# Optimization experiments

Hardware: AMD Instinct MI355X
Metric: run time of the kernel (lower is better)

## Reference

```python
import jax, jax.numpy as jnp
import numpy as np

B, H, S, D = 2, 8, 2048, 64


def setup_inputs() -> dict:
    key = jax.random.key(0)
    kq, kk, kv, km = jax.random.split(key, 4)
    Q = jax.random.normal(kq, (B, H, S, D), dtype=jnp.float32)
    K = jax.random.normal(kk, (B, H, S, D), dtype=jnp.float32)
    V = jax.random.normal(kv, (B, H, S, D), dtype=jnp.float32)
    attn_mask = jax.random.randint(km, (B, H, S, S), 0, 2).astype(jnp.bool_)
    return {"Q": Q, "K": K, "V": V, "attn_mask": attn_mask}


def reference(Q, K, V, attn_mask):
    # a = Q K^T / sqrt(D)
    scale = 1.0 / jnp.sqrt(jnp.float32(Q.shape[-1]))
    a = jnp.einsum("bhqd,bhkd->bhqk", Q, K) * scale
    a = jnp.where(attn_mask, jnp.float32(-1e9), a)
    attn_p = jax.nn.softmax(a, axis=-1)
    # FAITHFUL to source bug: uses pre-softmax scores `a`, not attn_p
    attn_v = jnp.einsum("bhqk,bhkd->bhqd", a, V)
    return attn_v, attn_p
```

## Files before the change

kernel.cpp:

```cpp
#include <hip/hip_runtime.h>
#include <hip/hip_bf16.h>


#define SS   2048
#define DD   64
#define NT   8
#define MASK_B 0
#define K_B    4224
#define V_B    6400
#define ARENA_H 8960
#define KST 68
#define VST 20
#define FST 132

#define OV_F4 524288
#define ZB_F4 8192
#define PK_OFF  131072
#define PK_BYTES ((size_t)16*2048*16*16)

typedef _Float16 half4_t  __attribute__((ext_vector_type(4)));
typedef _Float16 half2_t  __attribute__((ext_vector_type(2)));
typedef short    short4_t __attribute__((ext_vector_type(4)));
typedef float    float4_t __attribute__((ext_vector_type(4)));
typedef int      int2_t   __attribute__((ext_vector_type(2)));
typedef unsigned uint2_t  __attribute__((ext_vector_type(2)));
typedef unsigned long long ulong2_t __attribute__((ext_vector_type(2)));

static __device__ __forceinline__ unsigned short f2bf_u(float f) {
  __hip_bfloat16 h = __float2bfloat16(f);
  return __builtin_bit_cast(unsigned short, h);
}
static __device__ __forceinline__ unsigned packh2(float a, float b) {
  union { half2_t h; unsigned u; } c;
  c.h.x = (_Float16)a; c.h.y = (_Float16)b;
  return c.u;
}

extern "C" __global__ __launch_bounds__(256)
void zero_k(float4_t* __restrict__ Ov, float4_t* __restrict__ Zb)
{
  const int i = blockIdx.x * 256 + threadIdx.x;
  const float4_t z = (float4_t){0.f, 0.f, 0.f, 0.f};
  if (i < OV_F4) Ov[i] = z;
  else           Zb[i - OV_F4] = z;
}

extern "C" __global__ __launch_bounds__(256, 1)
void attn_z_k(const float* __restrict__ Qg, const float* __restrict__ Kg,
              const float* __restrict__ Vg, const int* __restrict__ Mg,
              float* __restrict__ Og, float* __restrict__ Zg,
              unsigned long long* __restrict__ Wp, int do_pack)
{
  __shared__ alignas(16) unsigned short arena[ARENA_H];

  const int wg  = blockIdx.x;
  const int xcd = wg & 7;
  const int ii  = wg >> 3;
  const int bh  = 2 * xcd + (ii >> 9);
  const int rem = ii & 511;
  const int qg  = rem >> 4;
  const int kc  = rem & 15;

  const int tid  = threadIdx.x;
  const int w    = tid >> 6;
  const int lane = tid & 63;
  const int g    = lane >> 4;
  const int ql   = lane & 15;

  const int q0 = qg * 64 + w * 16;
  const int k0 = kc * 128;

  const int krow = 4 * w + (lane >> 4);
  const int kcol = 4 * (lane & 15);

  const float* Kst = Kg + ((size_t)bh * SS + k0 + krow) * DD + kcol;
  const float* Vst = Vg + ((size_t)bh * SS + k0 + krow) * DD + kcol;

  float4_t qr[4];
  #pragma unroll
  for (int c = 0; c < 4; ++c)
    qr[c] = *(const float4_t*)(Qg + ((size_t)bh * SS + q0 + ql) * DD + 16 * c + 4 * g);

  int2_t mrow[16];
  #pragma unroll
  for (int r = 0; r < 16; ++r)
    mrow[r] = __builtin_nontemporal_load(
        (const int2_t*)(Mg + ((size_t)bh * SS + q0 + r) * SS + k0) + lane);

  float4_t kreg = *(const float4_t*)(Kst);
  float4_t vreg = *(const float4_t*)(Vst);

  half4_t qf[4];
  #pragma unroll
  for (int c = 0; c < 4; ++c) {
    half4_t h; h.x=(_Float16)qr[c].x; h.y=(_Float16)qr[c].y;
               h.z=(_Float16)qr[c].z; h.w=(_Float16)qr[c].w;
    qf[c] = h;
  }

  #pragma unroll
  for (int r = 0; r < 16; ++r) {
    const unsigned short pk =
        (unsigned short)((mrow[r].x ? 1u : 0u) | ((mrow[r].y ? 1u : 0u) << 8));
    arena[MASK_B + w * 1056 + r * 66 + lane] = pk;
    const unsigned long long ev = __ballot(mrow[r].x != 0);
    const unsigned long long od = __ballot(mrow[r].y != 0);
    if (do_pack && lane == 0) {
      ulong2_t pm; pm.x = ev; pm.y = od;
      *(ulong2_t*)&Wp[(((size_t)bh * SS + q0 + r) * 16 + kc) * 2] = pm;
    }
  }

  {
    half4_t kh; kh.x=(_Float16)kreg.x; kh.y=(_Float16)kreg.y;
                kh.z=(_Float16)kreg.z; kh.w=(_Float16)kreg.w;
    *(half4_t*)&arena[K_B + krow * KST + kcol] = kh;
    arena[V_B + (kcol + 0) * VST + krow] = f2bf_u(vreg.x);
    arena[V_B + (kcol + 1) * VST + krow] = f2bf_u(vreg.y);
    arena[V_B + (kcol + 2) * VST + krow] = f2bf_u(vreg.z);
    arena[V_B + (kcol + 3) * VST + krow] = f2bf_u(vreg.w);
  }
  __syncthreads();

  float4_t accO[4];
  #pragma unroll
  for (int c = 0; c < 4; ++c) accO[c] = (float4_t){0.f, 0.f, 0.f, 0.f};
  float zs = 0.f;

  const unsigned short NEGu = 0xCE6Eu;

  #pragma unroll
  for (int t = 0; t < NT; ++t) {
    const int s = t & 1;

    if (t + 1 < NT) {
      kreg = *(const float4_t*)(Kst + (size_t)16 * (t + 1) * DD);
      vreg = *(const float4_t*)(Vst + (size_t)16 * (t + 1) * DD);
    }

    half4_t kf[4];
    #pragma unroll
    for (int c = 0; c < 4; ++c)
      kf[c] = *(const half4_t*)&arena[K_B + s * 1088 + ql * KST + 16 * c + 4 * g];

    short4_t vf[4];
    #pragma unroll
    for (int c = 0; c < 4; ++c)
      vf[c] = *(const short4_t*)&arena[V_B + s * 1280 + (16 * c + ql) * VST + 4 * g];

    const unsigned mdw = *(const unsigned*)((const unsigned char*)arena
                          + 2u * (MASK_B + w * 1056 + ql * 66) + 16 * t + 4 * g);

    float4_t acc = (float4_t){0.f, 0.f, 0.f, 0.f};
    #pragma unroll
    for (int c = 0; c < 4; ++c)
      acc = __builtin_amdgcn_mfma_f32_16x16x16f16(kf[c], qf[c], acc, 0, 0, 0);

    const float a0 = (mdw & 0x000000ffu) ? -1e9f : acc.x * 0.125f;
    const float a1 = (mdw & 0x0000ff00u) ? -1e9f : acc.y * 0.125f;
    const float a2 = (mdw & 0x00ff0000u) ? -1e9f : acc.z * 0.125f;
    const float a3 = (mdw & 0xff000000u) ? -1e9f : acc.w * 0.125f;

    const float e0 = __expf(a0), e1 = __expf(a1);
    const float e2 = __expf(a2), e3 = __expf(a3);
    zs += (e0 + e1) + (e2 + e3);

    short4_t af;
    af.x = (short)((mdw & 0x000000ffu) ? NEGu : 0);
    af.y = (short)((mdw & 0x0000ff00u) ? NEGu : 0);
    af.z = (short)((mdw & 0x00ff0000u) ? NEGu : 0);
    af.w = (short)((mdw & 0xff000000u) ? NEGu : 0);
    #pragma unroll
    for (int c = 0; c < 4; ++c)
      accO[c] = __builtin_amdgcn_mfma_f32_16x16x16bf16_1k(af, vf[c], accO[c], 0, 0, 0);

    if (t + 1 < NT) {
      const int s2 = s ^ 1;
      half4_t kh; kh.x=(_Float16)kreg.x; kh.y=(_Float16)kreg.y;
                  kh.z=(_Float16)kreg.z; kh.w=(_Float16)kreg.w;
      *(half4_t*)&arena[K_B + s2 * 1088 + krow * KST + kcol] = kh;
      arena[V_B + s2 * 1280 + (kcol + 0) * VST + krow] = f2bf_u(vreg.x);
      arena[V_B + s2 * 1280 + (kcol + 1) * VST + krow] = f2bf_u(vreg.y);
      arena[V_B + s2 * 1280 + (kcol + 2) * VST + krow] = f2bf_u(vreg.z);
      arena[V_B + s2 * 1280 + (kcol + 3) * VST + krow] = f2bf_u(vreg.w);
    }
    __syncthreads();
  }

  zs += __shfl_xor(zs, 16);
  zs += __shfl_xor(zs, 32);
  if (lane < 16) atomicAdd(&Zg[(size_t)bh * SS + q0 + lane], zs);

  #pragma unroll
  for (int c = 0; c < 4; ++c) {
    float* op = Og + ((size_t)bh * SS + q0 + 4 * g) * DD + 16 * c + ql;
    atomicAdd(op + 0 * DD, accO[c].x);
    atomicAdd(op + 1 * DD, accO[c].y);
    atomicAdd(op + 2 * DD, accO[c].z);
    atomicAdd(op + 3 * DD, accO[c].w);
  }
}

extern "C" __global__ __launch_bounds__(256, 1)
void attn_p_pk(const float* __restrict__ Qg, const float* __restrict__ Kg,
               const float* __restrict__ Zg, const unsigned long long* __restrict__ Wp,
               float* __restrict__ Pg)
{
  __shared__ alignas(16) unsigned short arena[ARENA_H];

  const int wg  = blockIdx.x;
  const int xcd = wg & 7;
  const int ii  = wg >> 3;
  const int bh  = 2 * xcd + (ii >> 9);
  const int rem = ii & 511;
  const int qg  = rem >> 4;
  const int kc  = rem & 15;

  const int tid  = threadIdx.x;
  const int w    = tid >> 6;
  const int lane = tid & 63;
  const int g    = lane >> 4;
  const int ql   = lane & 15;

  const int q0 = qg * 64 + w * 16;
  const int k0 = kc * 128;

  const int krow = 4 * w + (lane >> 4);
  const int kcol = 4 * (lane & 15);

  const float* Kst = Kg + ((size_t)bh * SS + k0 + krow) * DD + kcol;

  float4_t qr[4];
  #pragma unroll
  for (int c = 0; c < 4; ++c)
    qr[c] = *(const float4_t*)(Qg + ((size_t)bh * SS + q0 + ql) * DD + 16 * c + 4 * g);

  const ulong2_t pm = *(const ulong2_t*)&Wp[(((size_t)bh * SS + q0 + ql) * 16 + kc) * 2];
  const unsigned long long ev = pm.x, od = pm.y;

  float4_t kreg = *(const float4_t*)(Kst);
  const float invZ = 1.0f / Zg[(size_t)bh * SS + q0 + ql];

  half4_t qf[4];
  #pragma unroll
  for (int c = 0; c < 4; ++c) {
    half4_t h; h.x=(_Float16)qr[c].x; h.y=(_Float16)qr[c].y;
               h.z=(_Float16)qr[c].z; h.w=(_Float16)qr[c].w;
    qf[c] = h;
  }

  {
    half4_t kh; kh.x=(_Float16)kreg.x; kh.y=(_Float16)kreg.y;
                kh.z=(_Float16)kreg.z; kh.w=(_Float16)kreg.w;
    *(half4_t*)&arena[K_B + krow * KST + kcol] = kh;
  }
  __syncthreads();

  unsigned e_dw[NT][2];

  #pragma unroll
  for (int t = 0; t < NT; ++t) {
    const int s = t & 1;

    if (t + 1 < NT)
      kreg = *(const float4_t*)(Kst + (size_t)16 * (t + 1) * DD);

    half4_t kf[4];
    #pragma unroll
    for (int c = 0; c < 4; ++c)
      kf[c] = *(const half4_t*)&arena[K_B + s * 1088 + ql * KST + 16 * c + 4 * g];

    float4_t acc = (float4_t){0.f, 0.f, 0.f, 0.f};
    #pragma unroll
    for (int c = 0; c < 4; ++c)
      acc = __builtin_amdgcn_mfma_f32_16x16x16f16(kf[c], qf[c], acc, 0, 0, 0);

    const int sh = 8 * t + 2 * g;
    const unsigned m0 = (unsigned)(ev >> sh) & 1u;
    const unsigned m1 = (unsigned)(od >> sh) & 1u;
    const unsigned m2 = (unsigned)(ev >> (sh + 1)) & 1u;
    const unsigned m3 = (unsigned)(od >> (sh + 1)) & 1u;

    const float a0 = m0 ? -1e9f : acc.x * 0.125f;
    const float a1 = m1 ? -1e9f : acc.y * 0.125f;
    const float a2 = m2 ? -1e9f : acc.z * 0.125f;
    const float a3 = m3 ? -1e9f : acc.w * 0.125f;

    const float p0 = __expf(a0) * invZ, p1 = __expf(a1) * invZ;
    const float p2 = __expf(a2) * invZ, p3 = __expf(a3) * invZ;
    e_dw[t][0] = packh2(p0, p1);
    e_dw[t][1] = packh2(p2, p3);

    if (t + 1 < NT) {
      const int s2 = s ^ 1;
      half4_t kh; kh.x=(_Float16)kreg.x; kh.y=(_Float16)kreg.y;
                  kh.z=(_Float16)kreg.z; kh.w=(_Float16)kreg.w;
      *(half4_t*)&arena[K_B + s2 * 1088 + krow * KST + kcol] = kh;
    }
    __syncthreads();
  }

  {
    unsigned short* Fw = arena + w * 2112;
    #pragma unroll
    for (int t = 0; t < NT; ++t) {
      uint2_t pk; pk.x = e_dw[t][0]; pk.y = e_dw[t][1];
      *(uint2_t*)&Fw[ql * FST + 16 * t + 4 * g] = pk;
    }
    asm volatile("s_waitcnt lgkmcnt(0)" ::: "memory");
    const size_t prow = (size_t)bh * SS + q0;
    #pragma unroll
    for (int rr = 0; rr < 8; ++rr) {
      const int row = 2 * rr + (lane >> 5);
      const half4_t ev4 = *(const half4_t*)&Fw[row * FST + 4 * (lane & 31)];
      float4_t pv;
      pv.x = (float)ev4.x; pv.y = (float)ev4.y; pv.z = (float)ev4.z; pv.w = (float)ev4.w;
      __builtin_nontemporal_store(pv, (float4_t*)(Pg + (prow + row) * SS + k0 + 4 * (lane & 31)));
    }
  }
}

extern "C" __global__ __launch_bounds__(256, 1)
void attn_p_dir(const float* __restrict__ Qg, const float* __restrict__ Kg,
                const int* __restrict__ Mg, const float* __restrict__ Zg,
                float* __restrict__ Pg)
{
  __shared__ alignas(16) unsigned short arena[ARENA_H];

  const int wg  = blockIdx.x;
  const int xcd = wg & 7;
  const int ii  = wg >> 3;
  const int bh  = 2 * xcd + (ii >> 9);
  const int rem = ii & 511;
  const int qg  = rem >> 4;
  const int kc  = rem & 15;

  const int tid  = threadIdx.x;
  const int w    = tid >> 6;
  const int lane = tid & 63;
  const int g    = lane >> 4;
  const int ql   = lane & 15;

  const int q0 = qg * 64 + w * 16;
  const int k0 = kc * 128;

  const int krow = 4 * w + (lane >> 4);
  const int kcol = 4 * (lane & 15);

  const float* Kst = Kg + ((size_t)bh * SS + k0 + krow) * DD + kcol;

  float4_t qr[4];
  #pragma unroll
  for (int c = 0; c < 4; ++c)
    qr[c] = *(const float4_t*)(Qg + ((size_t)bh * SS + q0 + ql) * DD + 16 * c + 4 * g);

  int2_t mrow[16];
  #pragma unroll
  for (int r = 0; r < 16; ++r)
    mrow[r] = *((const int2_t*)(Mg + ((size_t)bh * SS + q0 + r) * SS + k0) + lane);

  float4_t kreg = *(const float4_t*)(Kst);
  const float invZ = 1.0f / Zg[(size_t)bh * SS + q0 + ql];

  half4_t qf[4];
  #pragma unroll
  for (int c = 0; c < 4; ++c) {
    half4_t h; h.x=(_Float16)qr[c].x; h.y=(_Float16)qr[c].y;
               h.z=(_Float16)qr[c].z; h.w=(_Float16)qr[c].w;
    qf[c] = h;
  }

  #pragma unroll
  for (int r = 0; r < 16; ++r) {
    const unsigned short pk =
        (unsigned short)((mrow[r].x ? 1u : 0u) | ((mrow[r].y ? 1u : 0u) << 8));
    arena[MASK_B + w * 1056 + r * 66 + lane] = pk;
  }
  {
    half4_t kh; kh.x=(_Float16)kreg.x; kh.y=(_Float16)kreg.y;
                kh.z=(_Float16)kreg.z; kh.w=(_Float16)kreg.w;
    *(half4_t*)&arena[K_B + krow * KST + kcol] = kh;
  }
  __syncthreads();

  unsigned e_dw[NT][2];

  #pragma unroll
  for (int t = 0; t < NT; ++t) {
    const int s = t & 1;

    if (t + 1 < NT)
      kreg = *(const float4_t*)(Kst + (size_t)16 * (t + 1) * DD);

    half4_t kf[4];
    #pragma unroll
    for (int c = 0; c < 4; ++c)
      kf[c] = *(const half4_t*)&arena[K_B + s * 1088 + ql * KST + 16 * c + 4 * g];

    const unsigned mdw = *(const unsigned*)((const unsigned char*)arena
                          + 2u * (MASK_B + w * 1056 + ql * 66) + 16 * t + 4 * g);

    float4_t acc = (float4_t){0.f, 0.f, 0.f, 0.f};
    #pragma unroll
    for (int c = 0; c < 4; ++c)
      acc = __builtin_amdgcn_mfma_f32_16x16x16f16(kf[c], qf[c], acc, 0, 0, 0);

    const float a0 = (mdw & 0x000000ffu) ? -1e9f : acc.x * 0.125f;
    const float a1 = (mdw & 0x0000ff00u) ? -1e9f : acc.y * 0.125f;
    const float a2 = (mdw & 0x00ff0000u) ? -1e9f : acc.z * 0.125f;
    const float a3 = (mdw & 0xff000000u) ? -1e9f : acc.w * 0.125f;

    const float p0 = __expf(a0) * invZ, p1 = __expf(a1) * invZ;
    const float p2 = __expf(a2) * invZ, p3 = __expf(a3) * invZ;
    e_dw[t][0] = packh2(p0, p1);
    e_dw[t][1] = packh2(p2, p3);

    if (t + 1 < NT) {
      const int s2 = s ^ 1;
      half4_t kh; kh.x=(_Float16)kreg.x; kh.y=(_Float16)kreg.y;
                  kh.z=(_Float16)kreg.z; kh.w=(_Float16)kreg.w;
      *(half4_t*)&arena[K_B + s2 * 1088 + krow * KST + kcol] = kh;
    }
    __syncthreads();
  }

  {
    unsigned short* Fw = arena + w * 2112;
    #pragma unroll
    for (int t = 0; t < NT; ++t) {
      uint2_t pk; pk.x = e_dw[t][0]; pk.y = e_dw[t][1];
      *(uint2_t*)&Fw[ql * FST + 16 * t + 4 * g] = pk;
    }
    asm volatile("s_waitcnt lgkmcnt(0)" ::: "memory");
    const size_t prow = (size_t)bh * SS + q0;
    #pragma unroll
    for (int rr = 0; rr < 8; ++rr) {
      const int row = 2 * rr + (lane >> 5);
      const half4_t ev4 = *(const half4_t*)&Fw[row * FST + 4 * (lane & 31)];
      float4_t pv;
      pv.x = (float)ev4.x; pv.y = (float)ev4.y; pv.z = (float)ev4.z; pv.w = (float)ev4.w;
      __builtin_nontemporal_store(pv, (float4_t*)(Pg + (prow + row) * SS + k0 + 4 * (lane & 31)));
    }
  }
}

extern "C" void kernel_launch(void* const* d_in, const int* in_sizes, int n_in,
                              void* d_out, int out_size, void* d_ws, size_t ws_size,
                              hipStream_t stream) {
  const float* Q = (const float*)d_in[0];
  const float* K = (const float*)d_in[1];
  const float* V = (const float*)d_in[2];
  const int*   M = (const int*)d_in[3];
  float* Ov = (float*)d_out;
  float* P  = (float*)d_out + (size_t)2 * 8 * 2048 * 64;
  float* Zb = (float*)d_ws;
  unsigned long long* Wp = (unsigned long long*)((char*)d_ws + PK_OFF);
  const int packed = (ws_size >= PK_OFF + PK_BYTES) ? 1 : 0;

  zero_k<<<dim3((OV_F4 + ZB_F4) / 256), dim3(256), 0, stream>>>((float4_t*)Ov, (float4_t*)Zb);
  attn_z_k<<<dim3(8192), dim3(256), 0, stream>>>(Q, K, V, M, Ov, Zb, Wp, packed);
  if (packed)
    attn_p_pk<<<dim3(8192), dim3(256), 0, stream>>>(Q, K, Zb, Wp, P);
  else
    attn_p_dir<<<dim3(8192), dim3(256), 0, stream>>>(Q, K, M, Zb, P);
}
```

Baseline: 198.5 us.

## Restructure attn_z kernel so each wave owns its own key slice with LDS reduction

The attn_z_k kernel now gives each workgroup one 16-query tile and four waves that each process a separate 128-key slice, staging K/V per wave in a larger LDS arena with no per-step __syncthreads. Partial Z sums and output accumulators are reduced across waves in LDS before one set of global atomics. The goal is to remove per-iteration block barriers and cut global atomic traffic on O and Z by a factor of four. In exchange it uses more LDS, gives each workgroup less Q reuse, and loads K/V redundantly per wave. The remaining kernels are mostly renamed loop variables.

```diff
diff --git a/kernel.cpp b/kernel.cpp
--- a/kernel.cpp
+++ b/kernel.cpp
@@ -5,12 +5,15 @@
 #define SS   2048
 #define DD   64
 #define NT   8
+#define ZMB  0
+#define ZKB  4224
+#define ZVB  12928
+#define ZRZ  23168
+#define ZAH  23296
 #define MASK_B 0
 #define K_B    4224
-#define V_B    6400
 #define ARENA_H 8960
 #define KST 68
-#define VST 20
 #define FST 132
 
 #define OV_F4 524288
@@ -51,6 +54,192 @@
               float* __restrict__ Og, float* __restrict__ Zg,
               unsigned long long* __restrict__ Wp, int do_pack)
 {
+  __shared__ alignas(16) unsigned short arena[ZAH];
+
+  const int wg  = blockIdx.x;
+  const int xcd = wg & 7;
+  const int ii  = wg >> 3;
+  const int bh  = 2 * xcd + (ii >> 9);
+  const int rem = ii & 511;
+  const int qg  = rem >> 2;
+  const int kc  = rem & 3;
+
+  const int tid  = threadIdx.x;
+  const int w    = tid >> 6;
+  const int lane = tid & 63;
+  const int g    = lane >> 4;
+  const int ql   = lane & 15;
+
+  const int q0 = qg * 16;
+  const int kw = kc * 512 + w * 128;
+
+  const int srow = lane >> 4;
+  const int scol = 4 * (lane & 15);
+
+  const float* Kst = Kg + ((size_t)bh * SS + kw) * DD;
+  const float* Vst = Vg + ((size_t)bh * SS + kw) * DD;
+
+  float4_t qr[4];
+  #pragma unroll
+  for (int d = 0; d < 4; ++d)
+    qr[d] = *(const float4_t*)(Qg + ((size_t)bh * SS + q0 + ql) * DD + 16 * d + 4 * g);
+
+  int2_t mrow[16];
+  #pragma unroll
+  for (int r = 0; r < 16; ++r)
+    mrow[r] = __builtin_nontemporal_load(
+        (const int2_t*)(Mg + ((size_t)bh * SS + q0 + r) * SS + kw) + lane);
+
+  float4_t kr4[4], vr4[4];
+  #pragma unroll
+  for (int j = 0; j < 4; ++j) {
+    kr4[j] = *(const float4_t*)(Kst + (size_t)(4 * j + srow) * DD + scol);
+    vr4[j] = *(const float4_t*)(Vst + (size_t)(4 * j + srow) * DD + scol);
+  }
+
+  half4_t qf[4];
+  #pragma unroll
+  for (int d = 0; d < 4; ++d) {
+    half4_t h; h.x=(_Float16)qr[d].x; h.y=(_Float16)qr[d].y;
+               h.z=(_Float16)qr[d].z; h.w=(_Float16)qr[d].w;
+    qf[d] = h;
+  }
+
+  #pragma unroll
+  for (int r = 0; r < 16; ++r) {
+    const unsigned short pk =
+        (unsigned short)((mrow[r].x ? 1u : 0u) | ((mrow[r].y ? 1u : 0u) << 8));
+    arena[ZMB + w * 1056 + r * 66 + lane] = pk;
+    const unsigned long long ev = __ballot(mrow[r].x != 0);
+    const unsigned long long od = __ballot(mrow[r].y != 0);
+    if (do_pack && lane == 0) {
+      ulong2_t pm; pm.x = ev; pm.y = od;
+      *(ulong2_t*)&Wp[(((size_t)bh * SS + q0 + r) * 16 + kc * 4 + w) * 2] = pm;
+    }
+  }
+
+  #pragma unroll
+  for (int j = 0; j < 4; ++j) {
+    half4_t kh; kh.x=(_Float16)kr4[j].x; kh.y=(_Float16)kr4[j].y;
+                kh.z=(_Float16)kr4[j].z; kh.w=(_Float16)kr4[j].w;
+    *(half4_t*)&arena[ZKB + w * 2176 + (4 * j + srow) * 68 + scol] = kh;
+    arena[ZVB + w * 2560 + (scol + 0) * 20 + 4 * j + srow] = f2bf_u(vr4[j].x);
+    arena[ZVB + w * 2560 + (scol + 1) * 20 + 4 * j + srow] = f2bf_u(vr4[j].y);
+    arena[ZVB + w * 2560 + (scol + 2) * 20 + 4 * j + srow] = f2bf_u(vr4[j].z);
+    arena[ZVB + w * 2560 + (scol + 3) * 20 + 4 * j + srow] = f2bf_u(vr4[j].w);
+  }
+
+  float4_t accO[4];
+  #pragma unroll
+  for (int d = 0; d < 4; ++d) accO[d] = (float4_t){0.f, 0.f, 0.f, 0.f};
+  float zs = 0.f;
+
+  const unsigned short NEGu = 0xCE6Eu;
+
+  #pragma unroll
+  for (int t = 0; t < NT; ++t) {
+    const int s = t & 1;
+
+    if (t + 1 < NT) {
+      #pragma unroll
+      for (int j = 0; j < 4; ++j) {
+        kr4[j] = *(const float4_t*)(Kst + (size_t)(16 * (t + 1) + 4 * j + srow) * DD + scol);
+        vr4[j] = *(const float4_t*)(Vst + (size_t)(16 * (t + 1) + 4 * j + srow) * DD + scol);
+      }
+    }
+
+    half4_t kf[4];
+    #pragma unroll
+    for (int d = 0; d < 4; ++d)
+      kf[d] = *(const half4_t*)&arena[ZKB + w * 2176 + s * 1088 + ql * 68 + 16 * d + 4 * g];
+
+    short4_t vf[4];
+    #pragma unroll
+    for (int d = 0; d < 4; ++d)
+      vf[d] = *(const short4_t*)&arena[ZVB + w * 2560 + s * 1280 + (16 * d + ql) * 20 + 4 * g];
+
+    const unsigned mdw = *(const unsigned*)((const unsigned char*)arena
+                          + 2u * (ZMB + w * 1056 + ql * 66) + 16 * t + 4 * g);
+
+    float4_t acc = (float4_t){0.f, 0.f, 0.f, 0.f};
+    #pragma unroll
+    for (int d = 0; d < 4; ++d)
+      acc = __builtin_amdgcn_mfma_f32_16x16x16f16(kf[d], qf[d], acc, 0, 0, 0);
+
+    const float a0 = (mdw & 0x000000ffu) ? -1e9f : acc.x * 0.125f;
+    const float a1 = (mdw & 0x0000ff00u) ? -1e9f : acc.y * 0.125f;
+    const float a2 = (mdw & 0x00ff0000u) ? -1e9f : acc.z * 0.125f;
+    const float a3 = (mdw & 0xff000000u) ? -1e9f : acc.w * 0.125f;
+
+    const float e0 = __expf(a0), e1 = __expf(a1);
+    const float e2 = __expf(a2), e3 = __expf(a3);
+    zs += (e0 + e1) + (e2 + e3);
+
+    short4_t af;
+    af.x = (short)((mdw & 0x000000ffu) ? NEGu : 0);
+    af.y = (short)((mdw & 0x0000ff00u) ? NEGu : 0);
+    af.z = (short)((mdw & 0x00ff0000u) ? NEGu : 0);
+    af.w = (short)((mdw & 0xff000000u) ? NEGu : 0);
+    #pragma unroll
+    for (int d = 0; d < 4; ++d)
+      accO[d] = __builtin_amdgcn_mfma_f32_16x16x16bf16_1k(af, vf[d], accO[d], 0, 0, 0);
+
+    if (t + 1 < NT) {
+      const int s2 = s ^ 1;
+      #pragma unroll
+      for (int j = 0; j < 4; ++j) {
+        half4_t kh; kh.x=(_Float16)kr4[j].x; kh.y=(_Float16)kr4[j].y;
+                    kh.z=(_Float16)kr4[j].z; kh.w=(_Float16)kr4[j].w;
+        *(half4_t*)&arena[ZKB + w * 2176 + s2 * 1088 + (4 * j + srow) * 68 + scol] = kh;
+        arena[ZVB + w * 2560 + s2 * 1280 + (scol + 0) * 20 + 4 * j + srow] = f2bf_u(vr4[j].x);
+        arena[ZVB + w * 2560 + s2 * 1280 + (scol + 1) * 20 + 4 * j + srow] = f2bf_u(vr4[j].y);
+        arena[ZVB + w * 2560 + s2 * 1280 + (scol + 2) * 20 + 4 * j + srow] = f2bf_u(vr4[j].z);
+        arena[ZVB + w * 2560 + s2 * 1280 + (scol + 3) * 20 + 4 * j + srow] = f2bf_u(vr4[j].w);
+      }
+    }
+  }
+
+  zs += __shfl_xor(zs, 16);
+  zs += __shfl_xor(zs, 32);
+  float* redzf = (float*)&arena[ZRZ];
+  if (lane < 16) redzf[w * 16 + ql] = zs;
+
+  float* oflw = (float*)&arena[ZKB + w * 2176];
+  #pragma unroll
+  for (int d = 0; d < 4; ++d) {
+    oflw[(4 * g + 0) * 68 + 16 * d + ql] = accO[d].x;
+    oflw[(4 * g + 1) * 68 + 16 * d + ql] = accO[d].y;
+    oflw[(4 * g + 2) * 68 + 16 * d + ql] = accO[d].z;
+    oflw[(4 * g + 3) * 68 + 16 * d + ql] = accO[d].w;
+  }
+  __syncthreads();
+
+  if (w == 0 && lane < 16) {
+    const float Z = (redzf[ql] + redzf[16 + ql]) + (redzf[32 + ql] + redzf[48 + ql]);
+    atomicAdd(&Zg[(size_t)bh * SS + q0 + ql], Z);
+  }
+  {
+    const int row = tid >> 4;
+    const int col = 4 * (tid & 15);
+    float4_t sA = (float4_t){0.f, 0.f, 0.f, 0.f};
+    #pragma unroll
+    for (int W = 0; W < 4; ++W) {
+      const float4_t t4 = *(const float4_t*)((const float*)&arena[ZKB + W * 2176] + row * 68 + col);
+      sA.x += t4.x; sA.y += t4.y; sA.z += t4.z; sA.w += t4.w;
+    }
+    float* op = Og + ((size_t)bh * SS + q0 + row) * DD + col;
+    atomicAdd(op + 0, sA.x);
+    atomicAdd(op + 1, sA.y);
+    atomicAdd(op + 2, sA.z);
+    atomicAdd(op + 3, sA.w);
+  }
+}
+
+extern "C" __global__ __launch_bounds__(256, 1)
+void attn_p_pk(const float* __restrict__ Qg, const float* __restrict__ Kg,
+               const float* __restrict__ Zg, const unsigned long long* __restrict__ Wp,
+               float* __restrict__ Pg)
+{
   __shared__ alignas(16) unsigned short arena[ARENA_H];
 
   const int wg  = blockIdx.x;
@@ -74,137 +263,101 @@
   const int kcol = 4 * (lane & 15);
 
   const float* Kst = Kg + ((size_t)bh * SS + k0 + krow) * DD + kcol;
-  const float* Vst = Vg + ((size_t)bh * SS + k0 + krow) * DD + kcol;
 
   float4_t qr[4];
   #pragma unroll
-  for (int c = 0; c < 4; ++c)
-    qr[c] = *(const float4_t*)(Qg + ((size_t)bh * SS + q0 + ql) * DD + 16 * c + 4 * g);
-
-  int2_t mrow[16];
-  #pragma unroll
-  for (int r = 0; r < 16; ++r)
-    mrow[r] = __builtin_nontemporal_load(
-        (const int2_t*)(Mg + ((size_t)bh * SS + q0 + r) * SS + k0) + lane);
+  for (int d = 0; d < 4; ++d)
+    qr[d] = *(const float4_t*)(Qg + ((size_t)bh * SS + q0 + ql) * DD + 16 * d + 4 * g);
+
+  const ulong2_t pm = *(const ulong2_t*)&Wp[(((size_t)bh * SS + q0 + ql) * 16 + kc) * 2];
+  const unsigned long long ev = pm.x, od = pm.y;
 
   float4_t kreg = *(const float4_t*)(Kst);
-  float4_t vreg = *(const float4_t*)(Vst);
+  const float invZ = 1.0f / Zg[(size_t)bh * SS + q0 + ql];
 
   half4_t qf[4];
   #pragma unroll
-  for (int c = 0; c < 4; ++c) {
-    half4_t h; h.x=(_Float16)qr[c].x; h.y=(_Float16)qr[c].y;
-               h.z=(_Float16)qr[c].z; h.w=(_Float16)qr[c].w;
-    qf[c] = h;
-  }
-
-  #pragma unroll
-  for (int r = 0; r < 16; ++r) {
-    const unsigned short pk =
-        (unsigned short)((mrow[r].x ? 1u : 0u) | ((mrow[r].y ? 1u : 0u) << 8));
-    arena[MASK_B + w * 1056 + r * 66 + lane] = pk;
-    const unsigned long long ev = __ballot(mrow[r].x != 0);
-    const unsigned long long od = __ballot(mrow[r].y != 0);
-    if (do_pack && lane == 0) {
-      ulong2_t pm; pm.x = ev; pm.y = od;
-      *(ulong2_t*)&Wp[(((size_t)bh * SS + q0 + r) * 16 + kc) * 2] = pm;
-    }
+  for (int d = 0; d < 4; ++d) {
+    half4_t h; h.x=(_Float16)qr[d].x; h.y=(_Float16)qr[d].y;
+               h.z=(_Float16)qr[d].z; h.w=(_Float16)qr[d].w;
+    qf[d] = h;
   }
 
   {
     half4_t kh; kh.x=(_Float16)kreg.x; kh.y=(_Float16)kreg.y;
                 kh.z=(_Float16)kreg.z; kh.w=(_Float16)kreg.w;
     *(half4_t*)&arena[K_B + krow * KST + kcol] = kh;
-    arena[V_B + (kcol + 0) * VST + krow] = f2bf_u(vreg.x);
-    arena[V_B + (kcol + 1) * VST + krow] = f2bf_u(vreg.y);
-    arena[V_B + (kcol + 2) * VST + krow] = f2bf_u(vreg.z);
-    arena[V_B + (kcol + 3) * VST + krow] = f2bf_u(vreg.w);
   }
   __syncthreads();
 
-  float4_t accO[4];
-  #pragma unroll
-  for (int c = 0; c < 4; ++c) accO[c] = (float4_t){0.f, 0.f, 0.f, 0.f};
-  float zs = 0.f;
-
-  const unsigned short NEGu = 0xCE6Eu;
+  unsigned e_dw[NT][2];
 
   #pragma unroll
   for (int t = 0; t < NT; ++t) {
     const int s = t & 1;
 
-    if (t + 1 < NT) {
+    if (t + 1 < NT)
       kreg = *(const float4_t*)(Kst + (size_t)16 * (t + 1) * DD);
-      vreg = *(const float4_t*)(Vst + (size_t)16 * (t + 1) * DD);
-    }
 
     half4_t kf[4];
     #pragma unroll
-    for (int c = 0; c < 4; ++c)
-      kf[c] = *(const half4_t*)&arena[K_B + s * 1088 + ql * KST + 16 * c + 4 * g];
-
-    short4_t vf[4];
-    #pragma unroll
-    for (int c = 0; c < 4; ++c)
-      vf[c] = *(const short4_t*)&arena[V_B + s * 1280 + (16 * c + ql) * VST + 4 * g];
-
-    const unsigned mdw = *(const unsigned*)((const unsigned char*)arena
-                          + 2u * (MASK_B + w * 1056 + ql * 66) + 16 * t + 4 * g);
+    for (int d = 0; d < 4; ++d)
+      kf[d] = *(const half4_t*)&arena[K_B + s * 1088 + ql * KST + 16 * d + 4 * g];
 
     float4_t acc = (float4_t){0.f, 0.f, 0.f, 0.f};
     #pragma unroll
-    for (int c = 0; c < 4; ++c)
-      acc = __builtin_amdgcn_mfma_f32_16x16x16f16(kf[c], qf[c], acc, 0, 0, 0);
-
-    const float a0 = (mdw & 0x000000ffu) ? -1e9f : acc.x * 0.125f;
-    const float a1 = (mdw & 0x0000ff00u) ? -1e9f : acc.y * 0.125f;
-    const float a2 = (mdw & 0x00ff0000u) ? -1e9f : acc.z * 0.125f;
-    const float a3 = (mdw & 0xff000000u) ? -1e9f : acc.w * 0.125f;
-
-    const float e0 = __expf(a0), e1 = __expf(a1);
-    const float e2 = __expf(a2), e3 = __expf(a3);
-    zs += (e0 + e1) + (e2 + e3);
-
-    short4_t af;
-    af.x = (short)((mdw & 0x000000ffu) ? NEGu : 0);
-    af.y = (short)((mdw & 0x0000ff00u) ? NEGu : 0);
-    af.z = (short)((mdw & 0x00ff0000u) ? NEGu : 0);
-    af.w = (short)((mdw & 0xff000000u) ? NEGu : 0);
-    #pragma unroll
-    for (int c = 0; c < 4; ++c)
-      accO[c] = __builtin_amdgcn_mfma_f32_16x16x16bf16_1k(af, vf[c], accO[c], 0, 0, 0);
+    for (int d = 0; d < 4; ++d)
+      acc = __builtin_amdgcn_mfma_f32_16x16x16f16(kf[d], qf[d], acc, 0, 0, 0);
+
+    const int sh = 8 * t + 2 * g;
+    const unsigned m0 = (unsigned)(ev >> sh) & 1u;
+    const unsigned m1 = (unsigned)(od >> sh) & 1u;
+    const unsigned m2 = (unsigned)(ev >> (sh + 1)) & 1u;
+    const unsigned m3 = (unsigned)(od >> (sh + 1)) & 1u;
+
+    const float a0 = m0 ? -1e9f : acc.x * 0.125f;
+    const float a1 = m1 ? -1e9f : acc.y * 0.125f;
+    const float a2 = m2 ? -1e9f : acc.z * 0.125f;
+    const float a3 = m3 ? -1e9f : acc.w * 0.125f;
+
+    const float p0 = __expf(a0) * invZ, p1 = __expf(a1) * invZ;
+    const float p2 = __expf(a2) * invZ, p3 = __expf(a3) * invZ;
+    e_dw[t][0] = packh2(p0, p1);
+    e_dw[t][1] = packh2(p2, p3);
 
     if (t + 1 < NT) {
       const int s2 = s ^ 1;
       half4_t kh; kh.x=(_Float16)kreg.x; kh.y=(_Float16)kreg.y;
                   kh.z=(_Float16)kreg.z; kh.w=(_Float16)kreg.w;
       *(half4_t*)&arena[K_B + s2 * 1088 + krow * KST + kcol] = kh;
-      arena[V_B + s2 * 1280 + (kcol + 0) * VST + krow] = f2bf_u(vreg.x);
-      arena[V_B + s2 * 1280 + (kcol + 1) * VST + krow] = f2bf_u(vreg.y);
-      arena[V_B + s2 * 1280 + (kcol + 2) * VST + krow] = f2bf_u(vreg.z);
-      arena[V_B + s2 * 1280 + (kcol + 3) * VST + krow] = f2bf_u(vreg.w);
     }
     __syncthreads();
   }
 
-  zs += __shfl_xor(zs, 16);
-  zs += __shfl_xor(zs, 32);
-  if (lane < 16) atomicAdd(&Zg[(size_t)bh * SS + q0 + lane], zs);
-
-  #pragma unroll
-  for (int c = 0; c < 4; ++c) {
-    float* op = Og + ((size_t)bh * SS + q0 + 4 * g) * DD + 16 * c + ql;
-    atomicAdd(op + 0 * DD, accO[c].x);
-    atomicAdd(op + 1 * DD, accO[c].y);
-    atomicAdd(op + 2 * DD, accO[c].z);
-    atomicAdd(op + 3 * DD, accO[c].w);
+  {
+    unsigned short* Fw = arena + w * 2112;
+    #pragma unroll
+    for (int t = 0; t < NT; ++t) {
+      uint2_t pk; pk.x = e_dw[t][0]; pk.y = e_dw[t][1];
+      *(uint2_t*)&Fw[ql * FST + 16 * t + 4 * g] = pk;
+    }
+    asm volatile("s_waitcnt lgkmcnt(0)" ::: "memory");
+    const size_t prow = (size_t)bh * SS + q0;
+    #pragma unroll
+    for (int rr = 0; rr < 8; ++rr) {
+      const int row = 2 * rr + (lane >> 5);
+      const half4_t ev4 = *(const half4_t*)&Fw[row * FST + 4 * (lane & 31)];
+      float4_t pv;
+      pv.x = (float)ev4.x; pv.y = (float)ev4.y; pv.z = (float)ev4.z; pv.w = (float)ev4.w;
+      __builtin_nontemporal_store(pv, (float4_t*)(Pg + (prow + row) * SS + k0 + 4 * (lane & 31)));
+    }
   }
 }
 
 extern "C" __global__ __launch_bounds__(256, 1)
-void attn_p_pk(const float* __restrict__ Qg, const float* __restrict__ Kg,
-               const float* __restrict__ Zg, const unsigned long long* __restrict__ Wp,
-               float* __restrict__ Pg)
+void attn_p_dir(const float* __restrict__ Qg, const float* __restrict__ Kg,
+                const int* __restrict__ Mg, const float* __restrict__ Zg,
+                float* __restrict__ Pg)
 {
   __shared__ alignas(16) unsigned short arena[ARENA_H];
 
@@ -232,23 +385,31 @@
 
   float4_t qr[4];
   #pragma unroll
-  for (int c = 0; c < 4; ++c)
-    qr[c] = *(const float4_t*)(Qg + ((size_t)bh * SS + q0 + ql) * DD + 16 * c + 4 * g);
-
-  const ulong2_t pm = *(const ulong2_t*)&Wp[(((size_t)bh * SS + q0 + ql) * 16 + kc) * 2];
-  const unsigned long long ev = pm.x, od = pm.y;
+  for (int d = 0; d < 4; ++d)
+    qr[d] = *(const float4_t*)(Qg + ((size_t)bh * SS + q0 + ql) * DD + 16 * d + 4 * g);
+
+  int2_t mrow[16];
+  #pragma unroll
+  for (int r = 0; r < 16; ++r)
+    mrow[r] = *((const int2_t*)(Mg + ((size_t)bh * SS + q0 + r) * SS + k0) + lane);
 
   float4_t kreg = *(const float4_t*)(Kst);
   const float invZ = 1.0f / Zg[(size_t)bh * SS + q0 + ql];
 
   half4_t qf[4];
   #pragma unroll
-  for (int c = 0; c < 4; ++c) {
-    half4_t h; h.x=(_Float16)qr[c].x; h.y=(_Float16)qr[c].y;
-               h.z=(_Float16)qr[c].z; h.w=(_Float16)qr[c].w;
-    qf[c] = h;
-  }
-
+  for (int d = 0; d < 4; ++d) {
+    half4_t h; h.x=(_Float16)qr[d].x; h.y=(_Float16)qr[d].y;
+               h.z=(_Float16)qr[d].z; h.w=(_Float16)qr[d].w;
+    qf[d] = h;
+  }
+
+  #pragma unroll
+  for (int r = 0; r < 16; ++r) {
+    const unsigned short pk =
+        (unsigned short)((mrow[r].x ? 1u : 0u) | ((mrow[r].y ? 1u : 0u) << 8));
+    arena[MASK_B + w * 1056 + r * 66 + lane] = pk;
+  }
   {
     half4_t kh; kh.x=(_Float16)kreg.x; kh.y=(_Float16)kreg.y;
                 kh.z=(_Float16)kreg.z; kh.w=(_Float16)kreg.w;
@@ -267,143 +428,16 @@
 
     half4_t kf[4];
     #pragma unroll
-    for (int c = 0; c < 4; ++c)
-      kf[c] = *(const half4_t*)&arena[K_B + s * 1088 + ql * KST + 16 * c + 4 * g];
-
-    float4_t acc = (float4_t){0.f, 0.f, 0.f, 0.f};
-    #pragma unroll
-    for (int c = 0; c < 4; ++c)
-      acc = __builtin_amdgcn_mfma_f32_16x16x16f16(kf[c], qf[c], acc, 0, 0, 0);
-
-    const int sh = 8 * t + 2 * g;
-    const unsigned m0 = (unsigned)(ev >> sh) & 1u;
-    const unsigned m1 = (unsigned)(od >> sh) & 1u;
-    const unsigned m2 = (unsigned)(ev >> (sh + 1)) & 1u;
-    const unsigned m3 = (unsigned)(od >> (sh + 1)) & 1u;
-
-    const float a0 = m0 ? -1e9f : acc.x * 0.125f;
-    const float a1 = m1 ? -1e9f : acc.y * 0.125f;
-    const float a2 = m2 ? -1e9f : acc.z * 0.125f;
-    const float a3 = m3 ? -1e9f : acc.w * 0.125f;
-
-    const float p0 = __expf(a0) * invZ, p1 = __expf(a1) * invZ;
-    const float p2 = __expf(a2) * invZ, p3 = __expf(a3) * invZ;
-    e_dw[t][0] = packh2(p0, p1);
-    e_dw[t][1] = packh2(p2, p3);
-
-    if (t + 1 < NT) {
-      const int s2 = s ^ 1;
-      half4_t kh; kh.x=(_Float16)kreg.x; kh.y=(_Float16)kreg.y;
-                  kh.z=(_Float16)kreg.z; kh.w=(_Float16)kreg.w;
-      *(half4_t*)&arena[K_B + s2 * 1088 + krow * KST + kcol] = kh;
-    }
-    __syncthreads();
-  }
-
-  {
-    unsigned short* Fw = arena + w * 2112;
-    #pragma unroll
-    for (int t = 0; t < NT; ++t) {
-      uint2_t pk; pk.x = e_dw[t][0]; pk.y = e_dw[t][1];
-      *(uint2_t*)&Fw[ql * FST + 16 * t + 4 * g] = pk;
-    }
-    asm volatile("s_waitcnt lgkmcnt(0)" ::: "memory");
-    const size_t prow = (size_t)bh * SS + q0;
-    #pragma unroll
-    for (int rr = 0; rr < 8; ++rr) {
-      const int row = 2 * rr + (lane >> 5);
-      const half4_t ev4 = *(const half4_t*)&Fw[row * FST + 4 * (lane & 31)];
-      float4_t pv;
-      pv.x = (float)ev4.x; pv.y = (float)ev4.y; pv.z = (float)ev4.z; pv.w = (float)ev4.w;
-      __builtin_nontemporal_store(pv, (float4_t*)(Pg + (prow + row) * SS + k0 + 4 * (lane & 31)));
-    }
-  }
-}
-
-extern "C" __global__ __launch_bounds__(256, 1)
-void attn_p_dir(const float* __restrict__ Qg, const float* __restrict__ Kg,
-                const int* __restrict__ Mg, const float* __restrict__ Zg,
-                float* __restrict__ Pg)
-{
-  __shared__ alignas(16) unsigned short arena[ARENA_H];
-
-  const int wg  = blockIdx.x;
-  const int xcd = wg & 7;
-  const int ii  = wg >> 3;
-  const int bh  = 2 * xcd + (ii >> 9);
-  const int rem = ii & 511;
-  const int qg  = rem >> 4;
-  const int kc  = rem & 15;
-
-  const int tid  = threadIdx.x;
-  const int w    = tid >> 6;
-  const int lane = tid & 63;
-  const int g    = lane >> 4;
-  const int ql   = lane & 15;
-
-  const int q0 = qg * 64 + w * 16;
-  const int k0 = kc * 128;
-
-  const int krow = 4 * w + (lane >> 4);
-  const int kcol = 4 * (lane & 15);
-
-  const float* Kst = Kg + ((size_t)bh * SS + k0 + krow) * DD + kcol;
-
-  float4_t qr[4];
-  #pragma unroll
-  for (int c = 0; c < 4; ++c)
-    qr[c] = *(const float4_t*)(Qg + ((size_t)bh * SS + q0 + ql) * DD + 16 * c + 4 * g);
-
-  int2_t mrow[16];
-  #pragma unroll
-  for (int r = 0; r < 16; ++r)
-    mrow[r] = *((const int2_t*)(Mg + ((size_t)bh * SS + q0 + r) * SS + k0) + lane);
-
-  float4_t kreg = *(const float4_t*)(Kst);
-  const float invZ = 1.0f / Zg[(size_t)bh * SS + q0 + ql];
-
-  half4_t qf[4];
-  #pragma unroll
-  for (int c = 0; c < 4; ++c) {
-    half4_t h; h.x=(_Float16)qr[c].x; h.y=(_Float16)qr[c].y;
-               h.z=(_Float16)qr[c].z; h.w=(_Float16)qr[c].w;
-    qf[c] = h;
-  }
-
-  #pragma unroll
-  for (int r = 0; r < 16; ++r) {
-    const unsigned short pk =
-        (unsigned short)((mrow[r].x ? 1u : 0u) | ((mrow[r].y ? 1u : 0u) << 8));
-    arena[MASK_B + w * 1056 + r * 66 + lane] = pk;
-  }
-  {
-    half4_t kh; kh.x=(_Float16)kreg.x; kh.y=(_Float16)kreg.y;
-                kh.z=(_Float16)kreg.z; kh.w=(_Float16)kreg.w;
-    *(half4_t*)&arena[K_B + krow * KST + kcol] = kh;
-  }
-  __syncthreads();
-
-  unsigned e_dw[NT][2];
-
-  #pragma unroll
-  for (int t = 0; t < NT; ++t) {
-    const int s = t & 1;
-
-    if (t + 1 < NT)
-      kreg = *(const float4_t*)(Kst + (size_t)16 * (t + 1) * DD);
-
-    half4_t kf[4];
-    #pragma unroll
-    for (int c = 0; c < 4; ++c)
-      kf[c] = *(const half4_t*)&arena[K_B + s * 1088 + ql * KST + 16 * c + 4 * g];
+    for (int d = 0; d < 4; ++d)
+      kf[d] = *(const half4_t*)&arena[K_B + s * 1088 + ql * KST + 16 * d + 4 * g];
 
     const unsigned mdw = *(const unsigned*)((const unsigned char*)arena
                           + 2u * (MASK_B + w * 1056 + ql * 66) + 16 * t + 4 * g);
 
     float4_t acc = (float4_t){0.f, 0.f, 0.f, 0.f};
     #pragma unroll
-    for (int c = 0; c < 4; ++c)
-      acc = __builtin_amdgcn_mfma_f32_16x16x16f16(kf[c], qf[c], acc, 0, 0, 0);
+    for (int d = 0; d < 4; ++d)
+      acc = __builtin_amdgcn_mfma_f32_16x16x16f16(kf[d], qf[d], acc, 0, 0, 0);
 
     const float a0 = (mdw & 0x000000ffu) ? -1e9f : acc.x * 0.125f;
     const float a1 = (mdw & 0x0000ff00u) ? -1e9f : acc.y * 0.125f;
```

Result: slower. 225.6 us (+13.6%).
